# Kernel tuning notes

Hardware: AMD Instinct MI355X
Metric: run time of the kernel (lower is better)

## Reference

```python
import jax, jax.numpy as jnp
import numpy as np

ALPHA = 0.5
SPLIT_RATIO = 0.5
NUM_HEADS = 12
LN_EPS = 1e-6


def _layernorm(x, g, b):
    m = x.mean(-1, keepdims=True)
    v = ((x - m) ** 2).mean(-1, keepdims=True)
    return (x - m) * jax.lax.rsqrt(v + LN_EPS) * g + b


def setup_inputs() -> dict:
    key = jax.random.key(0)
    ks = jax.random.split(key, 8)
    B, N1, C, L, Hm = 16, 197, 768, 4, 3072
    s = 0.02
    return {
        "x": jax.random.normal(ks[0], (B, N1, C), jnp.float32),
        "glb_cls_attn": jax.random.uniform(ks[1], (B, N1 - 1), jnp.float32),
        "split_w": jax.random.normal(ks[2], (C, 4 * C), jnp.float32) * s,
        "split_b": jnp.zeros((4 * C,), jnp.float32),
        "ln1_g": jnp.ones((L, C), jnp.float32),
        "ln1_b": jnp.zeros((L, C), jnp.float32),
        "qkv_w": jax.random.normal(ks[3], (L, C, 3 * C), jnp.float32) * s,
        "qkv_b": jnp.zeros((L, 3 * C), jnp.float32),
        "proj_w": jax.random.normal(ks[4], (L, C, C), jnp.float32) * s,
        "proj_b": jnp.zeros((L, C), jnp.float32),
        "ln2_g": jnp.ones((L, C), jnp.float32),
        "ln2_b": jnp.zeros((L, C), jnp.float32),
        "fc1_w": jax.random.normal(ks[5], (L, C, Hm), jnp.float32) * s,
        "fc1_b": jnp.zeros((L, Hm), jnp.float32),
        "fc2_w": jax.random.normal(ks[6], (L, Hm, C), jnp.float32) * s,
        "fc2_b": jnp.zeros((L, C), jnp.float32),
    }


def reference(x, glb_cls_attn, split_w, split_b, ln1_g, ln1_b, qkv_w, qkv_b,
              proj_w, proj_b, ln2_g, ln2_b, fc1_w, fc1_b, fc2_w, fc2_b):
    B, _, C = x.shape
    H = NUM_HEADS
    D = C // H
    scale = D ** -0.5

    # --- token split based on global cls attention importance ---
    cls_tok, tokens = x[:, :1], x[:, 1:]
    order = jnp.argsort(-glb_cls_attn, axis=1)  # descending importance
    tokens = jnp.take_along_axis(tokens, order[:, :, None], axis=1)
    n = tokens.shape[1]
    split_n = int(n * SPLIT_RATIO)
    st = tokens[:, :split_n] @ split_w + split_b          # [B, split_n, 4C]
    st = st.reshape(B, split_n * 4, C)                    # each token -> 4 tokens
    x = jnp.concatenate([cls_tok, st, tokens[:, split_n:]], axis=1)
    N = x.shape[1]
    glb = jnp.zeros((B, N - 1), x.dtype)

    def block(carry, p):
        x, g = carry
        g1, b1, qw, qb, pw, pb, g2, b2, w1, bb1, w2, bb2 = p
        h = _layernorm(x, g1, b1)
        qkv = (h @ qw + qb).reshape(B, N, 3, H, D).transpose(2, 0, 3, 1, 4)
        q, k, v = qkv[0], qkv[1], qkv[2]                  # [B,H,N,D]
        attn = jax.nn.softmax(jnp.einsum('bhnd,bhmd->bhnm', q, k) * scale, axis=-1)
        cls_attn = attn[:, :, 0, 1:].mean(axis=1)         # mean over heads, row 0
        o = jnp.einsum('bhnm,bhmd->bhnd', attn, v).transpose(0, 2, 1, 3).reshape(B, N, C)
        x = x + o @ pw + pb
        h2 = _layernorm(x, g2, b2)
        x = x + jax.nn.gelu(h2 @ w1 + bb1, approximate=False) @ w2 + bb2
        g = ALPHA * g + (1.0 - ALPHA) * cls_attn
        return (x, g), None

    (x, glb), _ = jax.lax.scan(
        block, (x, glb),
        (ln1_g, ln1_b, qkv_w, qkv_b, proj_w, proj_b,
         ln2_g, ln2_b, fc1_w, fc1_b, fc2_w, fc2_b))
    return x, glb
```

## Files before the change

kernel.cpp:

```cpp
#include <hip/hip_runtime.h>
#include <math.h>

typedef unsigned short u16;
typedef short s16x8 __attribute__((ext_vector_type(8)));
typedef float f32x4 __attribute__((ext_vector_type(4)));

#define BB 16
#define N1 197
#define NTOK 196
#define SPLITN 98
#define NN 491
#define CC 768
#define H3 2304
#define HM 3072
#define NH 12
#define NL 4
#define BN (BB*NN)
#define MSPLIT (BB*SPLITN)

__device__ __forceinline__ float b2f(u16 u) {
    union { unsigned int i; float f; } x; x.i = ((unsigned int)u) << 16; return x.f;
}
__device__ __forceinline__ u16 f2b(float f) {
    union { float f; unsigned int i; } x; x.f = f;
    unsigned int i = x.i;
    return (u16)((i + 0x7fffu + ((i >> 16) & 1u)) >> 16);
}
__device__ __forceinline__ float ldx(const void* p, long long i, int isf32) {
    return isf32 ? ((const float*)p)[i] : b2f(((const u16*)p)[i]);
}

__device__ __forceinline__ void gload_lds16(const u16* g, u16* l) {
    __builtin_amdgcn_global_load_lds(
        (const __attribute__((address_space(1))) unsigned int*)g,
        (__attribute__((address_space(3))) unsigned int*)l,
        16, 0, 0);
}

__global__ void detect_k(const void* __restrict__ ln1_g, int* __restrict__ flag) {
    unsigned int w = ((const unsigned int*)ln1_g)[0];
    *flag = (w == 0x3F800000u) ? 1 : 0;
}

__global__ void zero_out_k(u16* __restrict__ out, long long n) {
    long long idx = (long long)blockIdx.x * 256 + threadIdx.x;
    if (idx < n) out[idx] = 0;
}

__global__ void zero_glb_k(float* __restrict__ glb) {
    int idx = blockIdx.x * 256 + threadIdx.x;
    if (idx < BB * (NN - 1)) glb[idx] = 0.0f;
}

__global__ void sort_k(const void* __restrict__ g, int* __restrict__ order,
                       const int* __restrict__ dflag) {
    __shared__ float v[256];
    int isf32 = *dflag;
    int b = blockIdx.x, t = threadIdx.x;
    float vv = -1e30f;
    if (t < NTOK) {
        vv = ldx(g, (long long)b * NTOK + t, isf32);
        if (!(vv == vv)) vv = -1e30f;
    }
    v[t] = vv;
    __syncthreads();
    if (t < NTOK) {
        float mv = v[t]; int r = 0;
        for (int j = 0; j < NTOK; j++) {
            float vj = v[j];
            if (vj > mv || (vj == mv && j < t)) r++;
        }
        order[b * NTOK + r] = t;
    }
}

__device__ __forceinline__ int clamp_tok(int tok) {
    return (tok < 0) ? 0 : (tok > NTOK - 1 ? NTOK - 1 : tok);
}

__global__ void gather_split_k(const void* __restrict__ x_in, const int* __restrict__ order,
                               u16* __restrict__ Asp, const int* __restrict__ dflag) {
    int isf32 = *dflag;
    long long idx = (long long)blockIdx.x * 256 + threadIdx.x;
    if (idx >= (long long)MSPLIT * CC) return;
    int c = (int)(idx % CC); int m = (int)(idx / CC); int b = m / SPLITN, r = m % SPLITN;
    int tok = clamp_tok(order[b * NTOK + r]);
    Asp[idx] = f2b(ldx(x_in, ((long long)b * N1 + 1 + tok) * CC + c, isf32));
}

__global__ void build_x_k(const void* __restrict__ x_in, const u16* __restrict__ st,
                          const int* __restrict__ order, float* __restrict__ x,
                          const int* __restrict__ dflag) {
    int isf32 = *dflag;
    long long idx = (long long)blockIdx.x * 256 + threadIdx.x;
    if (idx >= (long long)BN * CC) return;
    int c = (int)(idx % CC);
    int m = (int)(idx / CC);
    int b = m / NN, pos = m % NN;
    float v;
    if (pos == 0) {
        v = ldx(x_in, (long long)b * N1 * CC + c, isf32);
    } else if (pos < 1 + 4 * SPLITN) {
        int tt = pos - 1; int r = tt >> 2, kq = tt & 3;
        v = b2f(st[((long long)b * SPLITN + r) * HM + kq * CC + c]);
    } else {
        int j = pos - (1 + 4 * SPLITN);
        int tok = clamp_tok(order[b * NTOK + SPLITN + j]);
        v = ldx(x_in, ((long long)b * N1 + 1 + tok) * CC + c, isf32);
    }
    x[idx] = v;
}

__global__ void transpose_off_k(const void* __restrict__ in, u16* __restrict__ out, int K, int N,
                                long long off, const int* __restrict__ dflag) {
    __shared__ u16 tile[32][33];
    int isf32 = *dflag;
    int n0 = blockIdx.x * 32, k0 = blockIdx.y * 32;
    int tx = threadIdx.x, ty = threadIdx.y;
    for (int i = ty; i < 32; i += 8)
        tile[i][tx] = f2b(ldx(in, off + (long long)(k0 + i) * N + n0 + tx, isf32));
    __syncthreads();
    for (int i = ty; i < 32; i += 8) out[(long long)(n0 + i) * K + k0 + tx] = tile[tx][i];
}

__global__ __launch_bounds__(256) void ln_k(const float* __restrict__ x, const void* __restrict__ g,
                                            const void* __restrict__ bgain, u16* __restrict__ h,
                                            int goff, const int* __restrict__ dflag) {
    __shared__ float sb[8];
    int isf32 = *dflag;
    int row = blockIdx.x, t = threadIdx.x;
    const float* xr = x + (long long)row * CC;
    float v0 = xr[t], v1 = xr[t + 256], v2 = xr[t + 512];
    float s = v0 + v1 + v2;
    for (int o = 32; o > 0; o >>= 1) s += __shfl_down(s, o, 64);
    int lane = t & 63, w = t >> 6;
    if (lane == 0) sb[w] = s;
    __syncthreads();
    float mean = (sb[0] + sb[1] + sb[2] + sb[3]) * (1.0f / 768.0f);
    float d0 = v0 - mean, d1 = v1 - mean, d2 = v2 - mean;
    float q = d0 * d0 + d1 * d1 + d2 * d2;
    for (int o = 32; o > 0; o >>= 1) q += __shfl_down(q, o, 64);
    if (lane == 0) sb[4 + w] = q;
    __syncthreads();
    float var = (sb[4] + sb[5] + sb[6] + sb[7]) * (1.0f / 768.0f);
    float rs = rsqrtf(var + 1e-6f);
    long long o0 = (long long)row * CC;
    h[o0 + t]       = f2b(d0 * rs * ldx(g, goff + t, isf32)       + ldx(bgain, goff + t, isf32));
    h[o0 + t + 256] = f2b(d1 * rs * ldx(g, goff + t + 256, isf32) + ldx(bgain, goff + t + 256, isf32));
    h[o0 + t + 512] = f2b(d2 * rs * ldx(g, goff + t + 512, isf32) + ldx(bgain, goff + t + 512, isf32));
}

template<int TBM, int TBN>
__global__ __launch_bounds__(256) void gemm_t(const u16* __restrict__ A, const u16* __restrict__ BT,
                                              const void* __restrict__ bias, int boff,
                                              void* __restrict__ out,
                                              int M, int N, int K, int mode,
                                              const int* __restrict__ dflag) {
    constexpr int WM = TBM / 2, WN = TBN / 2, FM = WM / 16, FN = WN / 16;
    constexpr int AI = TBM / 64;
    constexpr int BI = TBN / 64;
    __shared__ __align__(16) u16 As[2][TBM * 32];
    __shared__ __align__(16) u16 Bs[2][TBN * 32];
    int isf32 = *dflag;

    int gx = gridDim.x, gy = gridDim.y;
    int nwg = gx * gy;
    int bid0 = blockIdx.y * gx + blockIdx.x;
    int q = nwg >> 3, rr = nwg & 7;
    int xcd = bid0 & 7, sl = bid0 >> 3;
    int wg = (xcd < rr ? xcd * (q + 1) : rr * (q + 1) + (xcd - rr) * q) + sl;
    int by = wg % gy, bx = wg / gy;
    int m0 = bx * TBM, n0 = by * TBN;

    int t = threadIdx.x, wave = t >> 6, lane = t & 63;
    int wm = (wave >> 1) * WM, wn = (wave & 1) * WN;
    int fr = lane & 15, quad = lane >> 4;

    int srow = lane >> 2;
    int scol = ((lane & 3) ^ ((srow >> 1) & 3)) * 8;

    f32x4 acc[FM][FN];
#pragma unroll
    for (int i = 0; i < FM; i++)
#pragma unroll
        for (int j = 0; j < FN; j++) acc[i][j] = (f32x4){0.f, 0.f, 0.f, 0.f};

    const int nk = K >> 5;

    auto stage = [&](int buf, int k0) {
#pragma unroll
        for (int i = 0; i < AI; i++) {
            int r0 = wave * (TBM / 4) + i * 16;
            int row = m0 + r0 + srow;
            if (row > M - 1) row = M - 1;
            gload_lds16(&A[(long long)row * K + k0 + scol], &As[buf][r0 * 32]);
        }
#pragma unroll
        for (int i = 0; i < BI; i++) {
            int r0 = wave * (TBN / 4) + i * 16;
            gload_lds16(&BT[(long long)(n0 + r0 + srow) * K + k0 + scol], &Bs[buf][r0 * 32]);
        }
    };

    stage(0, 0);
    __syncthreads();
    int rofs = ((quad ^ ((fr >> 1) & 3)) * 8);
    for (int kt = 0; kt < nk; kt++) {
        int cur = kt & 1;
        if (kt + 1 < nk) stage(cur ^ 1, (kt + 1) << 5);
        s16x8 af[FM], bf2[FN];
#pragma unroll
        for (int i = 0; i < FM; i++)
            af[i] = *(const s16x8*)&As[cur][(wm + i * 16 + fr) * 32 + rofs];
#pragma unroll
        for (int j = 0; j < FN; j++)
            bf2[j] = *(const s16x8*)&Bs[cur][(wn + j * 16 + fr) * 32 + rofs];
#pragma unroll
        for (int i = 0; i < FM; i++)
#pragma unroll
            for (int j = 0; j < FN; j++)
                acc[i][j] = __builtin_amdgcn_mfma_f32_16x16x32_bf16(af[i], bf2[j], acc[i][j], 0, 0, 0);
        __syncthreads();
    }

#pragma unroll
    for (int i = 0; i < FM; i++) {
#pragma unroll
        for (int j = 0; j < FN; j++) {
#pragma unroll
            for (int r = 0; r < 4; r++) {
                int row = m0 + wm + i * 16 + quad * 4 + r;
                int col = n0 + wn + j * 16 + fr;
                if (row < M) {
                    float v = acc[i][j][r] + ldx(bias, boff + col, isf32);
                    long long idx = (long long)row * N + col;
                    if (mode == 1) ((u16*)out)[idx] = f2b(v);
                    else if (mode == 2) {
                        float gl = 0.5f * v * (1.0f + erff(v * 0.70710678118654752f));
                        ((u16*)out)[idx] = f2b(gl);
                    } else ((float*)out)[idx] += v;
                }
            }
        }
    }
}

__global__ __launch_bounds__(256, 2) void attn_mfma_k(const u16* __restrict__ qkv,
                                                      u16* __restrict__ o,
                                                      float* __restrict__ cls_partial, int b0,
                                                      int nbh) {
    int bid = blockIdx.x;
    int chunk = nbh >> 3;
    int xcd = bid & 7, s = bid >> 3;
    int qt = s & 7;
    int bh = xcd * chunk + (s >> 3);
    int lb = bh / NH, h = bh % NH;
    int i0 = qt * 64;
    int w = threadIdx.x >> 6, lane = threadIdx.x & 63;
    int fr = lane & 15, quad = lane >> 4;
    int fk = quad * 8;

    __shared__ __align__(16) u16 Qs[64][72];
    __shared__ __align__(16) u16 Ks[64][72];
    __shared__ __align__(16) u16 Vt[64][72];
    __shared__ __align__(16) u16 Pst[4][16][72];

    const long long rowbase = (long long)lb * NN * H3 + (long long)h * 64;

    {
        int t = threadIdx.x;
#pragma unroll
        for (int i = 0; i < 2; i++) {
            int e = t + i * 256;
            int r = e >> 3, c8 = (e & 7) * 8;
            uint4 v = make_uint4(0u, 0u, 0u, 0u);
            int qrow = i0 + r;
            if (qrow < NN) v = *(const uint4*)&qkv[rowbase + (long long)qrow * H3 + c8];
            *(uint4*)&Qs[r][c8] = v;
        }
    }
    __syncthreads();
    s16x8 aq0 = *(const s16x8*)&Qs[w * 16 + fr][fk];
    s16x8 aq1 = *(const s16x8*)&Qs[w * 16 + fr][32 + fk];

    f32x4 S[32];
#pragma unroll
    for (int i = 0; i < 32; i++) S[i] = (f32x4){0.f, 0.f, 0.f, 0.f};

#pragma unroll
    for (int kt = 0; kt < 8; kt++) {
        int tb = kt * 64;
        __syncthreads();
        {
            int t = threadIdx.x;
#pragma unroll
            for (int i = 0; i < 2; i++) {
                int e = t + i * 256;
                int r = e >> 3, c8 = (e & 7) * 8;
                uint4 v = make_uint4(0u, 0u, 0u, 0u);
                int krow = tb + r;
                if (krow < NN) v = *(const uint4*)&qkv[rowbase + (long long)krow * H3 + CC + c8];
                *(uint4*)&Ks[r][c8] = v;
            }
        }
        __syncthreads();
#pragma unroll
        for (int ct = 0; ct < 4; ct++) {
            s16x8 bk0 = *(const s16x8*)&Ks[ct * 16 + fr][fk];
            s16x8 bk1 = *(const s16x8*)&Ks[ct * 16 + fr][32 + fk];
            S[kt * 4 + ct] = __builtin_amdgcn_mfma_f32_16x16x32_bf16(aq0, bk0, S[kt * 4 + ct], 0, 0, 0);
            S[kt * 4 + ct] = __builtin_amdgcn_mfma_f32_16x16x32_bf16(aq1, bk1, S[kt * 4 + ct], 0, 0, 0);
        }
    }

    float mrow[4] = {-1e30f, -1e30f, -1e30f, -1e30f};
#pragma unroll
    for (int tl = 0; tl < 32; tl++) {
        int col = tl * 16 + fr;
        bool valid = col < NN;
#pragma unroll
        for (int r = 0; r < 4; r++) {
            float s2 = S[tl][r] * 0.125f;
            s2 = valid ? s2 : -1e30f;
            S[tl][r] = s2;
            mrow[r] = fmaxf(mrow[r], s2);
        }
    }
#pragma unroll
    for (int m = 1; m < 16; m <<= 1)
#pragma unroll
        for (int r = 0; r < 4; r++) mrow[r] = fmaxf(mrow[r], __shfl_xor(mrow[r], m, 64));
    float lrow[4] = {0.f, 0.f, 0.f, 0.f};
#pragma unroll
    for (int tl = 0; tl < 32; tl++)
#pragma unroll
        for (int r = 0; r < 4; r++) {
            float e = __expf(S[tl][r] - mrow[r]);
            S[tl][r] = e;
            lrow[r] += e;
        }
#pragma unroll
    for (int m = 1; m < 16; m <<= 1)
#pragma unroll
        for (int r = 0; r < 4; r++) lrow[r] += __shfl_xor(lrow[r], m, 64);
    float linv[4];
#pragma unroll
    for (int r = 0; r < 4; r++) linv[r] = 1.0f / lrow[r];

    if (qt == 0 && w == 0 && quad == 0) {
        long long cbase = (long long)((b0 + lb) * NH + h) * (NN - 1);
        float inv = linv[0];
#pragma unroll
        for (int tl = 0; tl < 32; tl++) {
            int col = tl * 16 + fr;
            if (col >= 1 && col < NN) cls_partial[cbase + col - 1] = S[tl][0] * inv;
        }
    }

    f32x4 O[4];
#pragma unroll
    for (int d = 0; d < 4; d++) O[d] = (f32x4){0.f, 0.f, 0.f, 0.f};
#pragma unroll
    for (int kt2 = 0; kt2 < 8; kt2++) {
        int vb = kt2 * 64;
        __syncthreads();
        {
            int t = threadIdx.x;
#pragma unroll
            for (int i = 0; i < 2; i++) {
                int e = t + i * 256;
                int r = e >> 3, c8 = (e & 7) * 8;
                uint4 v = make_uint4(0u, 0u, 0u, 0u);
                int vrow = vb + r;
                if (vrow < NN) v = *(const uint4*)&qkv[rowbase + (long long)vrow * H3 + 2 * CC + c8];
                union { uint4 u; u16 e8[8]; } tmp; tmp.u = v;
                int rblk = r >> 3, rin = r & 7;
#pragma unroll
                for (int j = 0; j < 8; j++) {
                    int row = c8 + j;
                    int cp = ((rblk ^ (row >> 3)) << 3) | rin;
                    Vt[row][cp] = tmp.e8[j];
                }
            }
        }
#pragma unroll
        for (int tt = 0; tt < 4; tt++) {
            int tl = kt2 * 4 + tt;
#pragma unroll
            for (int r = 0; r < 4; r++)
                Pst[w][quad * 4 + r][tt * 16 + fr] = f2b(S[tl][r]);
        }
        __syncthreads();
        s16x8 ap0 = *(const s16x8*)&Pst[w][fr][fk];
        s16x8 ap1 = *(const s16x8*)&Pst[w][fr][32 + fk];
#pragma unroll
        for (int dt = 0; dt < 4; dt++) {
            int row = dt * 16 + fr;
            int g = row >> 3;
            s16x8 bv0 = *(const s16x8*)&Vt[row][((quad ^ g) & 7) * 8];
            s16x8 bv1 = *(const s16x8*)&Vt[row][(((4 + quad) ^ g) & 7) * 8];
            O[dt] = __builtin_amdgcn_mfma_f32_16x16x32_bf16(ap0, bv0, O[dt], 0, 0, 0);
            O[dt] = __builtin_amdgcn_mfma_f32_16x16x32_bf16(ap1, bv1, O[dt], 0, 0, 0);
        }
    }

#pragma unroll
    for (int r = 0; r < 4; r++) {
        int qrow = i0 + w * 16 + quad * 4 + r;
        if (qrow < NN) {
            long long obase = ((long long)(b0 + lb) * NN + qrow) * CC + h * 64;
#pragma unroll
            for (int dt = 0; dt < 4; dt++)
                o[obase + dt * 16 + fr] = f2b(O[dt][r] * linv[r]);
        }
    }
}

__global__ void glb_update_k(const float* __restrict__ cls_partial, float* __restrict__ glb) {
    int idx = blockIdx.x * 256 + threadIdx.x;
    if (idx >= BB * (NN - 1)) return;
    int b = idx / (NN - 1), j = idx % (NN - 1);
    float s = 0;
    for (int h = 0; h < NH; h++) s += cls_partial[(long long)(b * NH + h) * (NN - 1) + j];
    glb[idx] = 0.5f * glb[idx] + 0.5f * (s / NH);
}

__global__ void finalize_k(const float* __restrict__ x, const float* __restrict__ glb,
                           void* __restrict__ out, const int* __restrict__ dflag) {
    int isf32 = *dflag;
    long long nx = (long long)BN * CC;
    long long nt = nx + (long long)BB * (NN - 1);
    long long idx = (long long)blockIdx.x * 256 + threadIdx.x;
    if (idx >= nt) return;
    float v = (idx < nx) ? x[idx] : glb[idx - nx];
    if (isf32) ((float*)out)[idx] = v;
    else ((u16*)out)[idx] = f2b(v);
}

static inline char* carve(char*& p, size_t bytes) {
    char* r = p;
    p += (bytes + 255) & ~(size_t)255;
    return r;
}
static inline size_t padb(size_t b) { return (b + 255) & ~(size_t)255; }

extern "C" void kernel_launch(void* const* d_in, const int* in_sizes, int n_in,
                              void* d_out, int out_size, void* d_ws, size_t ws_size,
                              hipStream_t stream) {
    const void* x_in    = d_in[0];
    const void* glb_in  = d_in[1];
    const void* split_w = d_in[2];
    const void* split_b = d_in[3];
    const void* ln1_g   = d_in[4];
    const void* ln1_b   = d_in[5];
    const void* qkv_w   = d_in[6];
    const void* qkv_b   = d_in[7];
    const void* proj_w  = d_in[8];
    const void* proj_b  = d_in[9];
    const void* ln2_g   = d_in[10];
    const void* ln2_b   = d_in[11];
    const void* fc1_w   = d_in[12];
    const void* fc1_b   = d_in[13];
    const void* fc2_w   = d_in[14];
    const void* fc2_b   = d_in[15];

    const size_t sz_x    = (size_t)BN * CC * 4;
    const size_t sz_h    = (size_t)BN * CC * 2;
    const size_t sz_wt   = (size_t)HM * CC * 2;
    const size_t sz_cls  = (size_t)BB * NH * (NN - 1) * 4;
    const size_t sz_glb  = (size_t)BB * (NN - 1) * 4;
    const size_t sz_ord  = (size_t)BB * NTOK * 4;

    const size_t rA = (size_t)BN * H3 * 2;
    const size_t rB = (size_t)(BN / 4) * HM * 2;
    const size_t rC = (size_t)MSPLIT * HM * 2;

    const size_t base = padb(sz_x) + padb(sz_h) + 2 * padb(sz_wt) + padb(sz_cls) +
                        padb(sz_glb) + padb(sz_ord) + 256;
    int tier; size_t rsz;
    if (ws_size >= base + padb(rA))      { tier = 0; rsz = rA; }
    else if (ws_size >= base + padb(rB)) { tier = 1; rsz = rB; }
    else if (ws_size >= base + padb(rC)) { tier = 2; rsz = rC; }
    else {
        zero_out_k<<<(int)(((long long)out_size + 255) / 256), 256, 0, stream>>>((u16*)d_out, (long long)out_size);
        return;
    }

    char* p = (char*)d_ws;
    float* x_f32   = (float*)carve(p, sz_x);
    u16* h_buf     = (u16*)carve(p, sz_h);
    u16* region1   = (u16*)carve(p, rsz);
    u16* wtA       = (u16*)carve(p, sz_wt);
    u16* wtB       = (u16*)carve(p, sz_wt);
    float* cls_par = (float*)carve(p, sz_cls);
    float* glb_f32 = (float*)carve(p, sz_glb);
    int* order     = (int*)carve(p, sz_ord);
    int* dflag     = (int*)carve(p, 256);
    u16* Asp       = wtB;

    auto gemm = [&](const u16* A, const u16* BT, const void* bias, int boff, void* out,
                    int M, int N, int K, int mode) {
        long long b128 = (long long)((M + 127) / 128) * (N / 128);
        if ((N & 127) == 0 && b128 >= 512)
            gemm_t<128, 128><<<dim3((M + 127) / 128, N / 128), 256, 0, stream>>>(
                A, BT, bias, boff, out, M, N, K, mode, dflag);
        else
            gemm_t<64, 64><<<dim3((M + 63) / 64, N / 64), 256, 0, stream>>>(
                A, BT, bias, boff, out, M, N, K, mode, dflag);
    };

    dim3 tb(32, 8);
    detect_k<<<1, 1, 0, stream>>>(ln1_g, dflag);
    zero_glb_k<<<(BB * (NN - 1) + 255) / 256, 256, 0, stream>>>(glb_f32);
    sort_k<<<BB, 256, 0, stream>>>(glb_in, order, dflag);
    gather_split_k<<<(MSPLIT * CC + 255) / 256, 256, 0, stream>>>(x_in, order, Asp, dflag);
    transpose_off_k<<<dim3(HM / 32, CC / 32), tb, 0, stream>>>(split_w, wtA, CC, HM, 0, dflag);
    gemm(Asp, wtA, split_b, 0, region1, MSPLIT, HM, CC, 1);
    build_x_k<<<(int)(((long long)BN * CC + 255) / 256), 256, 0, stream>>>(x_in, region1, order,
                                                                           x_f32, dflag);

    const int bch  = (tier == 0) ? BB : 4;
    const int nbch = BB / bch;
    const int matt = bch * NN;
    const int nbh  = bch * NH;
    const int nmch = (tier == 0) ? 2 : (tier == 1) ? 4 : 8;
    const int mch  = BN / nmch;

    for (int l = 0; l < NL; l++) {
        transpose_off_k<<<dim3(H3 / 32, CC / 32), tb, 0, stream>>>(qkv_w, wtA, CC, H3,
                                                                   (long long)l * CC * H3, dflag);
        ln_k<<<BN, 256, 0, stream>>>(x_f32, ln1_g, ln1_b, h_buf, l * CC, dflag);
        for (int bc = 0; bc < nbch; bc++) {
            const u16* Ain = h_buf + (long long)bc * matt * CC;
            gemm(Ain, wtA, qkv_b, l * H3, region1, matt, H3, CC, 1);
            attn_mfma_k<<<dim3(nbh * 8), 256, 0, stream>>>(region1, h_buf, cls_par, bc * bch, nbh);
        }
        glb_update_k<<<(BB * (NN - 1) + 255) / 256, 256, 0, stream>>>(cls_par, glb_f32);
        transpose_off_k<<<dim3(CC / 32, CC / 32), tb, 0, stream>>>(proj_w, wtA, CC, CC,
                                                                   (long long)l * CC * CC, dflag);
        gemm(h_buf, wtA, proj_b, l * CC, x_f32, BN, CC, CC, 3);
        ln_k<<<BN, 256, 0, stream>>>(x_f32, ln2_g, ln2_b, h_buf, l * CC, dflag);
        transpose_off_k<<<dim3(HM / 32, CC / 32), tb, 0, stream>>>(fc1_w, wtA, CC, HM,
                                                                   (long long)l * CC * HM, dflag);
        transpose_off_k<<<dim3(CC / 32, HM / 32), tb, 0, stream>>>(fc2_w, wtB, HM, CC,
                                                                   (long long)l * HM * CC, dflag);
        for (int mc = 0; mc < nmch; mc++) {
            const u16* Ain = h_buf + (long long)mc * mch * CC;
            float* xout    = x_f32 + (long long)mc * mch * CC;
            gemm(Ain, wtA, fc1_b, l * HM, region1, mch, HM, CC, 2);
            gemm(region1, wtB, fc2_b, l * CC, xout, mch, CC, HM, 3);
        }
    }
    long long total_out = (long long)BN * CC + (long long)BB * (NN - 1);
    finalize_k<<<(int)((total_out + 255) / 256), 256, 0, stream>>>(x_f32, glb_f32, d_out, dflag);
}
```

Baseline: 1.788 ms.

## Prefetch two k-tiles ahead in GEMM and run MLP unchunked when workspace allows

The GEMM main loop now issues the load for tile k+2 into the buffer just consumed, using explicit vmcnt waits and raw s_barriers in place of __syncthreads, so global-to-LDS loads get more time to overlap with MFMA work. A new top workspace tier sizes the intermediate region to hold the full fc1 output, so the MLP runs as one chunk instead of two. The price is an extra barrier per iteration, hand-counted vmcnt values that are only correct if gload_lds16 issues one load per call, and a larger workspace requirement for the new tier.

```diff
diff --git a/kernel.cpp b/kernel.cpp
--- a/kernel.cpp
+++ b/kernel.cpp
@@ -159,6 +159,7 @@
     constexpr int WM = TBM / 2, WN = TBN / 2, FM = WM / 16, FN = WN / 16;
     constexpr int AI = TBM / 64;
     constexpr int BI = TBN / 64;
+    constexpr int LPS = AI + BI;
     __shared__ __align__(16) u16 As[2][TBM * 32];
     __shared__ __align__(16) u16 Bs[2][TBN * 32];
     int isf32 = *dflag;
@@ -201,13 +202,25 @@
             gload_lds16(&BT[(long long)(n0 + r0 + srow) * K + k0 + scol], &Bs[buf][r0 * 32]);
         }
     };
+    auto wait_pf = [&](bool pf) {
+        if (pf) {
+            if constexpr (LPS == 4) asm volatile("s_waitcnt vmcnt(4)" ::: "memory");
+            else                    asm volatile("s_waitcnt vmcnt(2)" ::: "memory");
+        } else {
+            asm volatile("s_waitcnt vmcnt(0)" ::: "memory");
+        }
+    };
 
     stage(0, 0);
-    __syncthreads();
+    if (nk > 1) stage(1, 32);
+    wait_pf(nk > 1);
+    __builtin_amdgcn_sched_barrier(0);
+    __builtin_amdgcn_s_barrier();
+    __builtin_amdgcn_sched_barrier(0);
+
     int rofs = ((quad ^ ((fr >> 1) & 3)) * 8);
     for (int kt = 0; kt < nk; kt++) {
         int cur = kt & 1;
-        if (kt + 1 < nk) stage(cur ^ 1, (kt + 1) << 5);
         s16x8 af[FM], bf2[FN];
 #pragma unroll
         for (int i = 0; i < FM; i++)
@@ -220,7 +233,16 @@
 #pragma unroll
             for (int j = 0; j < FN; j++)
                 acc[i][j] = __builtin_amdgcn_mfma_f32_16x16x32_bf16(af[i], bf2[j], acc[i][j], 0, 0, 0);
-        __syncthreads();
+        if (kt + 1 >= nk) break;
+        __builtin_amdgcn_sched_barrier(0);
+        __builtin_amdgcn_s_barrier();
+        __builtin_amdgcn_sched_barrier(0);
+        bool pf = (kt + 2 < nk);
+        if (pf) stage(cur, (kt + 2) << 5);
+        wait_pf(pf);
+        __builtin_amdgcn_sched_barrier(0);
+        __builtin_amdgcn_s_barrier();
+        __builtin_amdgcn_sched_barrier(0);
     }
 
 #pragma unroll
@@ -471,16 +493,18 @@
     const size_t sz_glb  = (size_t)BB * (NN - 1) * 4;
     const size_t sz_ord  = (size_t)BB * NTOK * 4;
 
-    const size_t rA = (size_t)BN * H3 * 2;
-    const size_t rB = (size_t)(BN / 4) * HM * 2;
-    const size_t rC = (size_t)MSPLIT * HM * 2;
+    const size_t rA2 = (size_t)BN * HM * 2;
+    const size_t rA  = (size_t)BN * H3 * 2;
+    const size_t rB  = (size_t)(BN / 4) * HM * 2;
+    const size_t rC  = (size_t)MSPLIT * HM * 2;
 
     const size_t base = padb(sz_x) + padb(sz_h) + 2 * padb(sz_wt) + padb(sz_cls) +
                         padb(sz_glb) + padb(sz_ord) + 256;
     int tier; size_t rsz;
-    if (ws_size >= base + padb(rA))      { tier = 0; rsz = rA; }
-    else if (ws_size >= base + padb(rB)) { tier = 1; rsz = rB; }
-    else if (ws_size >= base + padb(rC)) { tier = 2; rsz = rC; }
+    if (ws_size >= base + padb(rA2))     { tier = 0; rsz = rA2; }
+    else if (ws_size >= base + padb(rA)) { tier = 1; rsz = rA; }
+    else if (ws_size >= base + padb(rB)) { tier = 2; rsz = rB; }
+    else if (ws_size >= base + padb(rC)) { tier = 3; rsz = rC; }
     else {
         zero_out_k<<<(int)(((long long)out_size + 255) / 256), 256, 0, stream>>>((u16*)d_out, (long long)out_size);
         return;
@@ -519,11 +543,11 @@
     build_x_k<<<(int)(((long long)BN * CC + 255) / 256), 256, 0, stream>>>(x_in, region1, order,
                                                                            x_f32, dflag);
 
-    const int bch  = (tier == 0) ? BB : 4;
+    const int bch  = (tier <= 1) ? BB : 4;
     const int nbch = BB / bch;
     const int matt = bch * NN;
     const int nbh  = bch * NH;
-    const int nmch = (tier == 0) ? 2 : (tier == 1) ? 4 : 8;
+    const int nmch = (tier == 0) ? 1 : (tier == 1) ? 2 : (tier == 2) ? 4 : 8;
     const int mch  = BN / nmch;
 
     for (int l = 0; l < NL; l++) {
```

New measurement: 1.708 ms. 4.5% less time.
